# Kernel optimization log

Measured on AMD Instinct MI355X. Metric: run time of the kernel, lower is better.

Reference implementation:

```python
import jax, jax.numpy as jnp
import numpy as np

C = 64      # in_channels
D = 64      # hidden_dim (= per-head out dim since concat=False)
H = 4       # heads
N1 = 20000
N2 = 20000
E = 320000
NEG_SLOPE = 0.2


def setup_inputs() -> dict:
    key = jax.random.key(0)
    ks = jax.random.split(key, 32)
    inp = {}
    inp['x1'] = jax.random.normal(ks[0], (N1, C), dtype=jnp.float32)
    inp['x2'] = jax.random.normal(ks[1], (N2, C), dtype=jnp.float32)
    inp['edge_index1'] = jax.random.randint(ks[2], (2, E), 0, N1, dtype=jnp.int64)
    inp['edge_index2'] = jax.random.randint(ks[3], (2, E), 0, N2, dtype=jnp.int64)
    i = 4
    for tag in ['0', '1', '2', 'f']:
        inp['W' + tag] = jax.random.normal(ks[i], (H * D, C), dtype=jnp.float32) / np.sqrt(C); i += 1
        inp['as' + tag] = jax.random.normal(ks[i], (H, D), dtype=jnp.float32) * 0.1; i += 1
        inp['ad' + tag] = jax.random.normal(ks[i], (H, D), dtype=jnp.float32) * 0.1; i += 1
        inp['b' + tag] = jax.random.normal(ks[i], (C,), dtype=jnp.float32) * 0.02; i += 1
    inp['Wr'] = jax.random.normal(ks[i], (C, C), dtype=jnp.float32) / np.sqrt(C); i += 1
    inp['br'] = jax.random.normal(ks[i], (C,), dtype=jnp.float32) * 0.02
    return inp


def _build_edges(edge_index1, edge_index2, n1, n2):
    """Eval-mode combined edge list: e1 | e2+n1 | e1+n1, coalesced (dedup),
    then self-loops replaced with the full set (PyG GATConv behavior).
    Host-side numpy since edge dedup is data-dependent."""
    e1 = np.asarray(edge_index1)
    e2 = np.asarray(edge_index2) + n1
    e1o = e1 + n1  # edge_manipulator eval path: offset then mask (always valid here)
    valid = (e1o[0] < n1 + n2) & (e1o[1] < n1 + n2)
    e1o = e1o[:, valid]
    comb = np.concatenate([e1, e2, e1o], axis=1)
    comb = np.unique(comb, axis=1)  # coalesce: sort + dedup
    n = n1 + n2
    comb = comb[:, comb[0] != comb[1]]  # remove self loops
    loops = np.arange(n, dtype=comb.dtype)
    src = np.concatenate([comb[0], loops])
    dst = np.concatenate([comb[1], loops])
    return jnp.asarray(src), jnp.asarray(dst)


def gat(h_in, src, dst, n, W, a_s, a_d, b):
    # PyG GATConv, concat=False: mean over heads, bias of size out_channels.
    h = (h_in @ W.T).reshape(n, H, -1)                    # [N,H,D]
    asrc = jnp.einsum('nhd,hd->nh', h, a_s)               # [N,H]
    adst = jnp.einsum('nhd,hd->nh', h, a_d)
    e = jax.nn.leaky_relu(asrc[src] + adst[dst], NEG_SLOPE)  # [E,H]
    m = jax.ops.segment_max(e, dst, num_segments=n)
    ex = jnp.exp(e - m[dst])
    s = jax.ops.segment_sum(ex, dst, num_segments=n)
    alpha = ex / (s[dst] + 1e-16)                         # segment softmax over in-edges
    out = jax.ops.segment_sum(alpha[:, :, None] * h[src], dst, num_segments=n)  # [N,H,D]
    return out.mean(axis=1) + b


def reference(x1, x2, edge_index1, edge_index2,
              W0, as0, ad0, b0, W1, as1, ad1, b1, W2, as2, ad2, b2,
              Wf, asf, adf, bf, Wr, br):
    n1, n2 = x1.shape[0], x2.shape[0]
    n = n1 + n2
    src, dst = _build_edges(edge_index1, edge_index2, n1, n2)

    residual = x2 @ Wr.T + br
    h = jnp.concatenate([x1, x2], axis=0)
    # stacked layers (run under no_grad in torch; same forward math, eval dropout = identity)
    for (W, a_s, a_d, b) in [(W0, as0, ad0, b0), (W1, as1, ad1, b1), (W2, as2, ad2, b2)]:
        h = jax.nn.relu(gat(h, src, dst, n, W, a_s, a_d, b))
    h = gat(h, src, dst, n, Wf, asf, adf, bf)

    h2 = h[n1:n1 + n2]
    norm = jnp.linalg.norm(h2, axis=1, keepdims=True)
    h2n = h2 / jnp.maximum(norm, 1e-12)  # F.normalize(p=2, dim=1)
    return h2n + residual
```

## Files before the change

kernel.cpp:

```cpp
#include <hip/hip_runtime.h>

#define N1V 20000
#define N2V 20000
#define NU  20000
#define NUP 20032
#define EV  320000
#define CAP 128
#define SCB ((NU + 255) / 256)
#define BMW 640

typedef _Float16 f16x8 __attribute__((ext_vector_type(8)));
typedef float    f32x4 __attribute__((ext_vector_type(4)));
typedef float    f32x2 __attribute__((ext_vector_type(2)));

__device__ __forceinline__ unsigned short f2h_bits(float f){
  return __builtin_bit_cast(unsigned short, (_Float16)f);
}

__device__ __forceinline__ unsigned char f2fp8(float f){
#if __has_builtin(__builtin_amdgcn_cvt_pk_fp8_f32)
  int pk = __builtin_amdgcn_cvt_pk_fp8_f32(f, 0.f, 0, false);
  return (unsigned char)(pk & 0xff);
#else
  float a = fabsf(f);
  unsigned sgn = (f < 0.f) ? 0x80u : 0u;
  if (!(a == a)) return (unsigned char)(sgn | 0x7f);
  if (a < 7.8125e-3f) return (unsigned char)sgn;
  if (a > 448.f) a = 448.f;
  unsigned u = __float_as_uint(a);
  int e = (int)((u >> 23) & 0xff) - 127;
  unsigned m = (u >> 20) & 7u;
  unsigned rest = u & 0xfffffu;
  if (rest > 0x80000u || (rest == 0x80000u && (m & 1u))){ m++; if (m == 8u){ m = 0u; e++; } }
  if (e < -6) return (unsigned char)sgn;
  if (e > 8){ e = 8; m = 7u; }
  return (unsigned char)(sgn | ((unsigned)(e + 7) << 3) | m);
#endif
}

template<bool HI>
__device__ __forceinline__ f32x2 fp8pair(unsigned v){
#if __has_builtin(__builtin_amdgcn_cvt_pk_f32_fp8)
  auto t = __builtin_amdgcn_cvt_pk_f32_fp8((int)v, HI);
  return __builtin_bit_cast(f32x2, t);
#else
  unsigned b0 = (v >> (HI ? 16 : 0)) & 0xffu, b1 = (v >> (HI ? 24 : 8)) & 0xffu;
  auto one = [](unsigned b)->float{
    unsigned s = b & 0x80u, ef = (b >> 3) & 15u, m = b & 7u;
    float mag = ef ? __uint_as_float(((ef + 120u) << 23) | (m << 20))
                   : (float)m * 0.001953125f;
    return s ? -mag : mag;
  };
  f32x2 r = {one(b0), one(b1)};
  return r;
#endif
}

__global__ __launch_bounds__(256) void zero_init(unsigned* __restrict__ c1,
                                                 unsigned* __restrict__ c2,
                                                 unsigned* __restrict__ flag){
  int i = blockIdx.x*256 + threadIdx.x;
  if (i < NU){ c1[i] = 0u; c2[i] = 0u; }
  if (i == 0) *flag = 0u;
}

__global__ void detect_dtype(const unsigned* __restrict__ e, unsigned* __restrict__ flag){
  unsigned v = e[2*threadIdx.x + 1];
  if (v) atomicOr(flag, 1u);
}

__device__ __forceinline__ int rd_idx(const void* p, long long i, bool is64){
  return is64 ? (int)((const long long*)p)[i] : ((const int*)p)[i];
}

__global__ void scatter_buckets(const void* e1, const void* e2, const unsigned* __restrict__ flag,
                                unsigned* __restrict__ c1, unsigned* __restrict__ c2,
                                unsigned short* __restrict__ bA, unsigned short* __restrict__ bB){
  int i = blockIdx.x*blockDim.x + threadIdx.x;
  if (i >= 2*EV) return;
  bool is64 = (*flag == 0u);
  if (i < EV){
    int s = rd_idx(e1, i, is64), d = rd_idx(e1, (long long)EV+i, is64);
    if (s != d){
      unsigned p1 = atomicAdd(&c1[d], 1u);
      if (p1 < CAP) bA[(size_t)d*CAP + p1] = (unsigned short)s;
    }
  } else {
    int j = i - EV;
    int s = rd_idx(e2, j, is64), d = rd_idx(e2, (long long)EV+j, is64);
    if (s != d){
      unsigned p2 = atomicAdd(&c2[d], 1u);
      if (p2 < CAP) bB[(size_t)d*CAP + p2] = (unsigned short)s;
    }
  }
}

__device__ __forceinline__ unsigned row_raw(const unsigned* c1, const unsigned* c2, int i){
  unsigned a = c1[i]; if (a > CAP) a = CAP;
  unsigned b = c2[i]; if (b > CAP) b = CAP;
  return a + b + 1u;
}

__global__ __launch_bounds__(256) void scan_part(const unsigned* __restrict__ c1,
                                                 const unsigned* __restrict__ c2,
                                                 unsigned* __restrict__ bsum){
  int i = blockIdx.x*256 + threadIdx.x;
  unsigned v = (i < NU) ? row_raw(c1, c2, i) : 0u;
  #pragma unroll
  for (int off=32; off; off>>=1) v += __shfl_xor((int)v, off);
  __shared__ unsigned ws4[4];
  if ((threadIdx.x & 63) == 0) ws4[threadIdx.x >> 6] = v;
  __syncthreads();
  if (threadIdx.x == 0) bsum[blockIdx.x] = ws4[0]+ws4[1]+ws4[2]+ws4[3];
}

__global__ __launch_bounds__(256) void scan_final(const unsigned* __restrict__ c1,
                                                  const unsigned* __restrict__ c2,
                                                  const unsigned* __restrict__ bsum,
                                                  unsigned* __restrict__ rowoff){
  __shared__ unsigned lds[256];
  __shared__ unsigned ws4[4];
  int b = blockIdx.x, t = threadIdx.x;
  unsigned bv = (t < b) ? bsum[t] : 0u;
  #pragma unroll
  for (int off=32; off; off>>=1) bv += __shfl_xor((int)bv, off);
  if ((t & 63) == 0) ws4[t >> 6] = bv;
  __syncthreads();
  unsigned base = ws4[0]+ws4[1]+ws4[2]+ws4[3];
  int i = b*256 + t;
  unsigned v = (i < NU) ? row_raw(c1, c2, i) : 0u;
  lds[t] = v; __syncthreads();
  #pragma unroll
  for (int off=1; off<256; off<<=1){
    unsigned x = (t >= off) ? lds[t-off] : 0u;
    __syncthreads();
    lds[t] += x;
    __syncthreads();
  }
  unsigned excl = lds[t] - v + base;
  if (i < NU) rowoff[i] = excl;
  if (i == NU-1) rowoff[NU] = excl + v;
}

__global__ __launch_bounds__(256) void dedup_rows(
    const unsigned short* __restrict__ bA, const unsigned short* __restrict__ bB,
    const unsigned* __restrict__ c1, const unsigned* __restrict__ c2,
    const unsigned* __restrict__ rowoff, unsigned* __restrict__ csr,
    unsigned* __restrict__ rowcnt)
{
  __shared__ unsigned bm[4][BMW];
  int w = threadIdx.x >> 6, lane = threadIdx.x & 63;
  int t = blockIdx.x*4 + w;
  unsigned* bmw = bm[w];
  #pragma unroll
  for (int i = lane; i < BMW; i += 64) bmw[i] = 0u;
  __syncthreads();

  unsigned b = rowoff[t];
  unsigned a = c1[t]; if (a > CAP) a = CAP;
  unsigned bb = c2[t]; if (bb > CAP) bb = CAP;
  int nA = (int)a, nB = (int)bb;
  const unsigned short* rA = &bA[(size_t)t*CAP];
  const unsigned short* rB = &bB[(size_t)t*CAP];
  int cnt = nA + nB;
  int wc = 0;
  for (int i0 = 0; i0 < cnt; i0 += 64){
    int i = i0 + lane;
    bool act = (i < cnt);
    unsigned v = 0u;
    if (act) v = (i < nA) ? (unsigned)rA[i] : (unsigned)rB[i - nA];
    bool keep = false;
    if (act){
      unsigned bit = 1u << (v & 31u);
      unsigned old = atomicOr(&bmw[v >> 5], bit);
      keep = (old & bit) == 0u;
    }
    unsigned long long mask = __ballot(keep);
    int pos = wc + (int)__popcll(mask & ((1ull << lane) - 1ull));
    if (keep) csr[b + (unsigned)pos] = v;
    wc += (int)__popcll(mask);
  }
  if (lane == 0){
    csr[b + (unsigned)wc] = (unsigned)t;
    rowcnt[t] = (unsigned)(wc + 1);
  }
}

__global__ __launch_bounds__(256) void gemm_hp(
    const float* __restrict__ hin, const float* __restrict__ x2,
    const float* __restrict__ W,
    const float* __restrict__ a_s, const float* __restrict__ a_d,
    unsigned char* __restrict__ hp8, float* __restrict__ asv, float* __restrict__ adv)
{
  __shared__ __align__(16) unsigned short As[64][72];
  __shared__ __align__(16) unsigned short Bs[256][72];
  int tid = threadIdx.x;
  int nb  = blockIdx.x * 64;
  for (int i = tid; i < 256*64; i += 256)
    Bs[i>>6][i&63] = f2h_bits(W[i]);
  const float* src = hin ? hin : x2;
  for (int i = tid; i < 64*64; i += 256){
    int r = i>>6, c = i&63;
    int gn = nb + r; if (gn >= NU) gn = NU-1;
    As[r][c] = f2h_bits(src[(size_t)gn*64 + c]);
  }
  __syncthreads();

  int w = tid >> 6, lane = tid & 63;
  int fr = lane & 15, fq = lane >> 4;
  int wc = w * 64;
  const f32x4 zero = {0.f, 0.f, 0.f, 0.f};
  f32x4 acc[4][4];
  #pragma unroll
  for (int a=0; a<4; ++a)
    #pragma unroll
    for (int b=0; b<4; ++b) acc[a][b] = zero;

  #pragma unroll
  for (int ks=0; ks<2; ++ks){
    int k0 = ks*32 + fq*8;
    f16x8 af[4], bfv[4];
    #pragma unroll
    for (int rt=0; rt<4; ++rt) af[rt]  = *(const f16x8*)&As[rt*16 + fr][k0];
    #pragma unroll
    for (int ct=0; ct<4; ++ct) bfv[ct] = *(const f16x8*)&Bs[wc + ct*16 + fr][k0];
    #pragma unroll
    for (int rt=0; rt<4; ++rt)
      #pragma unroll
      for (int ct=0; ct<4; ++ct)
        acc[rt][ct] = __builtin_amdgcn_mfma_f32_16x16x32_f16(af[rt], bfv[ct], acc[rt][ct], 0, 0, 0);
  }

  #pragma unroll
  for (int rt=0; rt<4; ++rt)
    #pragma unroll
    for (int ct=0; ct<4; ++ct)
      #pragma unroll
      for (int j=0; j<4; ++j){
        int gn = nb + rt*16 + fq*4 + j;
        int o  = wc + ct*16 + fr;
        hp8[(size_t)gn*256 + ((o & 63) << 2) + (o >> 6)] = f2fp8(acc[rt][ct][j]);
      }

  float asr[4], adr[4];
  #pragma unroll
  for (int ct=0; ct<4; ++ct){
    asr[ct] = a_s[wc + ct*16 + fr];
    adr[ct] = a_d[wc + ct*16 + fr];
  }
  #pragma unroll
  for (int rt=0; rt<4; ++rt)
    #pragma unroll
    for (int j=0; j<4; ++j){
      float ps = acc[rt][0][j]*asr[0] + acc[rt][1][j]*asr[1]
               + acc[rt][2][j]*asr[2] + acc[rt][3][j]*asr[3];
      float pd = acc[rt][0][j]*adr[0] + acc[rt][1][j]*adr[1]
               + acc[rt][2][j]*adr[2] + acc[rt][3][j]*adr[3];
      #pragma unroll
      for (int off=1; off<16; off<<=1){
        ps += __shfl_xor(ps, off);
        pd += __shfl_xor(pd, off);
      }
      if (fr == 0){
        int gn = nb + rt*16 + fq*4 + j;
        asv[(size_t)gn*4 + w] = ps;
        adv[(size_t)gn*4 + w] = pd;
      }
    }
}

template<int MODE>
__global__ __launch_bounds__(256) void gat_aggr8(
    const unsigned* __restrict__ csr, const unsigned* __restrict__ rowoff,
    const unsigned* __restrict__ rowcnt, const unsigned char* __restrict__ hp8,
    const float* __restrict__ asv, const float* __restrict__ adv,
    const float* __restrict__ bias, float* __restrict__ hout,
    const float* __restrict__ resid, float* __restrict__ outp)
{
  __shared__ __align__(16) float4 wbuf[4][64];
  int w    = threadIdx.x >> 6;
  int lane = threadIdx.x & 63;
  int dst  = blockIdx.x*4 + w;
  unsigned base = rowoff[dst];
  int cnt = (int)rowcnt[dst];
  float4 adn = *(const float4*)&adv[(size_t)dst*4];
  float4* wrow = wbuf[w];

  f32x2 accA = {0.f, 0.f}, accB = {0.f, 0.f};
  float ss0=0.f, ss1=0.f, ss2=0.f, ss3=0.f;

#define GATHER1(J) { \
    int su = __builtin_amdgcn_readlane(sv, (J)); \
    float4 wv = wrow[(J)]; \
    unsigned hv = *(const unsigned*)(hp8 + (((size_t)(unsigned)su) << 8) + (lane << 2)); \
    f32x2 h01 = fp8pair<false>(hv); \
    f32x2 h23 = fp8pair<true>(hv); \
    f32x2 w01 = {wv.x, wv.y}, w23 = {wv.z, wv.w}; \
    accA += h01 * w01; \
    accB += h23 * w23; }

  for (int i0=0; i0<cnt; i0+=64){
    int i = i0 + lane;
    int sv = 0; float x0=0.f, x1=0.f, x2v=0.f, x3=0.f;
    if (i < cnt){
      sv = (int)csr[base + i];
      float4 a = *(const float4*)&asv[(size_t)sv*4];
      float e0 = a.x + adn.x; e0 = e0 > 0.f ? e0 : 0.2f*e0; x0  = __expf(e0 - 4.f);
      float e1 = a.y + adn.y; e1 = e1 > 0.f ? e1 : 0.2f*e1; x1  = __expf(e1 - 4.f);
      float e2 = a.z + adn.z; e2 = e2 > 0.f ? e2 : 0.2f*e2; x2v = __expf(e2 - 4.f);
      float e3 = a.w + adn.w; e3 = e3 > 0.f ? e3 : 0.2f*e3; x3  = __expf(e3 - 4.f);
      ss0 += x0; ss1 += x1; ss2 += x2v; ss3 += x3;
    }
    float4 wpk = {x0, x1, x2v, x3};
    wrow[lane] = wpk;
    __builtin_amdgcn_wave_barrier();
    int lim = cnt - i0; if (lim > 64) lim = 64;
    int lim8 = (lim + 7) & ~7;
    for (int j = 0; j < lim8; j += 8){
      GATHER1(j)
      GATHER1(j+1)
      GATHER1(j+2)
      GATHER1(j+3)
      GATHER1(j+4)
      GATHER1(j+5)
      GATHER1(j+6)
      GATHER1(j+7)
    }
    __builtin_amdgcn_wave_barrier();
  }
#undef GATHER1

  #pragma unroll
  for (int off=32; off; off>>=1){
    ss0 += __shfl_xor(ss0, off); ss1 += __shfl_xor(ss1, off);
    ss2 += __shfl_xor(ss2, off); ss3 += __shfl_xor(ss3, off);
  }
  float r = 0.25f*( accA.x/(ss0 + 1e-16f) + accA.y/(ss1 + 1e-16f)
                  + accB.x/(ss2 + 1e-16f) + accB.y/(ss3 + 1e-16f) ) + bias[lane];
  if (MODE == 0){
    r = fmaxf(r, 0.f);
    hout[(size_t)dst*64 + lane] = r;
  } else {
    float ssq = r*r;
    #pragma unroll
    for (int off=32; off; off>>=1) ssq += __shfl_xor(ssq, off);
    float sc = 1.f / fmaxf(sqrtf(ssq), 1e-12f);
    size_t o = (size_t)dst*64 + lane;
    outp[o] = r*sc + resid[o];
  }
}

__global__ __launch_bounds__(256) void resid_gemm(const float* __restrict__ x2,
    const float* __restrict__ Wr, const float* __restrict__ br, float* __restrict__ resid){
  __shared__ float WT[64][65];
  int tid = threadIdx.x;
  for (int i = tid; i < 64*64; i += 256) WT[i & 63][i >> 6] = Wr[i];
  __syncthreads();
  int row = blockIdx.x*4 + (tid >> 6);
  int c   = tid & 63;
  const float* xr = &x2[(size_t)row*64];
  float acc = br[c];
  #pragma unroll 8
  for (int k=0; k<64; ++k) acc = fmaf(xr[k], WT[k][c], acc);
  resid[(size_t)row*64 + c] = acc;
}

extern "C" void kernel_launch(void* const* d_in, const int* in_sizes, int n_in,
                              void* d_out, int out_size, void* d_ws, size_t ws_size,
                              hipStream_t stream)
{
  (void)in_sizes; (void)n_in; (void)out_size; (void)ws_size;
  const float* x2  = (const float*)d_in[1];
  const void*  ei1 = d_in[2];
  const void*  ei2 = d_in[3];
  const float* Wm[4] = {(const float*)d_in[4],  (const float*)d_in[8],
                        (const float*)d_in[12], (const float*)d_in[16]};
  const float* Asv[4] = {(const float*)d_in[5],  (const float*)d_in[9],
                         (const float*)d_in[13], (const float*)d_in[17]};
  const float* Adv[4] = {(const float*)d_in[6],  (const float*)d_in[10],
                         (const float*)d_in[14], (const float*)d_in[18]};
  const float* Bv[4]  = {(const float*)d_in[7],  (const float*)d_in[11],
                         (const float*)d_in[15], (const float*)d_in[19]};
  const float* Wr = (const float*)d_in[20];
  const float* br = (const float*)d_in[21];
  float* out = (float*)d_out;

  char* p = (char*)d_ws;
  auto alloc = [&](size_t b){ void* r = (void*)p; p += (b + 1023) & ~(size_t)1023; return r; };
  unsigned* c1      = (unsigned*)alloc((size_t)NU*4);
  unsigned* c2      = (unsigned*)alloc((size_t)NU*4);
  unsigned* rowoff  = (unsigned*)alloc((size_t)(NU+1)*4);
  unsigned* rowcnt  = (unsigned*)alloc((size_t)NU*4);
  unsigned* bsum    = (unsigned*)alloc((size_t)SCB*4);
  unsigned* csr     = (unsigned*)alloc((size_t)(2*EV + NU)*4);
  unsigned short* bA = (unsigned short*)alloc((size_t)NU*CAP*2);
  unsigned short* bB = (unsigned short*)alloc((size_t)NU*CAP*2);
  unsigned char* hp8 = (unsigned char*)alloc((size_t)NUP*256);
  float* asv   = (float*)alloc((size_t)NUP*4*4);
  float* adv   = (float*)alloc((size_t)NUP*4*4);
  float* bufA  = (float*)alloc((size_t)NUP*64*4);
  float* bufB  = (float*)alloc((size_t)NUP*64*4);
  float* resid = (float*)alloc((size_t)N2V*64*4);
  unsigned* flag = (unsigned*)alloc(4);

  zero_init<<<SCB, 256, 0, stream>>>(c1, c2, flag);
  detect_dtype<<<1, 256, 0, stream>>>((const unsigned*)ei1, flag);
  scatter_buckets<<<(2*EV + 255)/256, 256, 0, stream>>>(ei1, ei2, flag, c1, c2, bA, bB);
  scan_part<<<SCB, 256, 0, stream>>>(c1, c2, bsum);
  scan_final<<<SCB, 256, 0, stream>>>(c1, c2, bsum, rowoff);
  dedup_rows<<<NU/4, 256, 0, stream>>>(bA, bB, c1, c2, rowoff, csr, rowcnt);
  resid_gemm<<<N2V/4, 256, 0, stream>>>(x2, Wr, br, resid);

  const float* hin = nullptr;
  float* houts[3] = {bufA, bufB, bufA};
  for (int l = 0; l < 3; ++l){
    gemm_hp<<<NUP/64, 256, 0, stream>>>(hin, x2, Wm[l], Asv[l], Adv[l], hp8, asv, adv);
    gat_aggr8<0><<<NU/4, 256, 0, stream>>>(csr, rowoff, rowcnt, hp8, asv, adv, Bv[l],
                                           houts[l], nullptr, nullptr);
    hin = houts[l];
  }
  gemm_hp<<<NUP/64, 256, 0, stream>>>(hin, x2, Wm[3], Asv[3], Adv[3], hp8, asv, adv);
  gat_aggr8<2><<<NU/4, 256, 0, stream>>>(csr, rowoff, rowcnt, hp8, asv, adv, Bv[3],
                                         nullptr, resid, out);
}
```

Measured before the change: 240.7 us.

## Replace CSR build with in-place deduped fixed-stride uint16 buckets

Drops the two prefix-scan kernels and the separate 32-bit CSR array. Each destination row now lives in a fixed-stride 16-bit bucket (272 slots) that is deduplicated in place, and the aggregation kernels read neighbor indices straight from it. The per-row counters are spaced 16 words apart to cut atomic contention on shared cache lines. This saves two kernel launches and halves the bytes per index read in the four aggregation passes. In exchange it uses a larger, padded bucket footprint, and a larger counter array must be zeroed.

Result: faster. 229.0 us (-4.9%).

```diff
diff --git a/kernel.cpp b/kernel.cpp
--- a/kernel.cpp
+++ b/kernel.cpp
@@ -6,7 +6,8 @@
 #define NUP 20032
 #define EV  320000
 #define CAP 128
-#define SCB ((NU + 255) / 256)
+#define CSTR 16
+#define BSTR 272
 #define BMW 640
 
 typedef _Float16 f16x8 __attribute__((ext_vector_type(8)));
@@ -60,7 +61,7 @@
                                                  unsigned* __restrict__ c2,
                                                  unsigned* __restrict__ flag){
   int i = blockIdx.x*256 + threadIdx.x;
-  if (i < NU){ c1[i] = 0u; c2[i] = 0u; }
+  if (i < NU*CSTR){ c1[i] = 0u; c2[i] = 0u; }
   if (i == 0) *flag = 0u;
 }
 
@@ -75,77 +76,29 @@
 
 __global__ void scatter_buckets(const void* e1, const void* e2, const unsigned* __restrict__ flag,
                                 unsigned* __restrict__ c1, unsigned* __restrict__ c2,
-                                unsigned short* __restrict__ bA, unsigned short* __restrict__ bB){
+                                unsigned short* __restrict__ bucket){
   int i = blockIdx.x*blockDim.x + threadIdx.x;
   if (i >= 2*EV) return;
   bool is64 = (*flag == 0u);
   if (i < EV){
     int s = rd_idx(e1, i, is64), d = rd_idx(e1, (long long)EV+i, is64);
     if (s != d){
-      unsigned p1 = atomicAdd(&c1[d], 1u);
-      if (p1 < CAP) bA[(size_t)d*CAP + p1] = (unsigned short)s;
+      unsigned p = atomicAdd(&c1[(size_t)d*CSTR], 1u);
+      if (p < CAP) bucket[(size_t)d*BSTR + p] = (unsigned short)s;
     }
   } else {
     int j = i - EV;
     int s = rd_idx(e2, j, is64), d = rd_idx(e2, (long long)EV+j, is64);
     if (s != d){
-      unsigned p2 = atomicAdd(&c2[d], 1u);
-      if (p2 < CAP) bB[(size_t)d*CAP + p2] = (unsigned short)s;
-    }
-  }
-}
-
-__device__ __forceinline__ unsigned row_raw(const unsigned* c1, const unsigned* c2, int i){
-  unsigned a = c1[i]; if (a > CAP) a = CAP;
-  unsigned b = c2[i]; if (b > CAP) b = CAP;
-  return a + b + 1u;
-}
-
-__global__ __launch_bounds__(256) void scan_part(const unsigned* __restrict__ c1,
-                                                 const unsigned* __restrict__ c2,
-                                                 unsigned* __restrict__ bsum){
-  int i = blockIdx.x*256 + threadIdx.x;
-  unsigned v = (i < NU) ? row_raw(c1, c2, i) : 0u;
-  #pragma unroll
-  for (int off=32; off; off>>=1) v += __shfl_xor((int)v, off);
-  __shared__ unsigned ws4[4];
-  if ((threadIdx.x & 63) == 0) ws4[threadIdx.x >> 6] = v;
-  __syncthreads();
-  if (threadIdx.x == 0) bsum[blockIdx.x] = ws4[0]+ws4[1]+ws4[2]+ws4[3];
-}
-
-__global__ __launch_bounds__(256) void scan_final(const unsigned* __restrict__ c1,
-                                                  const unsigned* __restrict__ c2,
-                                                  const unsigned* __restrict__ bsum,
-                                                  unsigned* __restrict__ rowoff){
-  __shared__ unsigned lds[256];
-  __shared__ unsigned ws4[4];
-  int b = blockIdx.x, t = threadIdx.x;
-  unsigned bv = (t < b) ? bsum[t] : 0u;
-  #pragma unroll
-  for (int off=32; off; off>>=1) bv += __shfl_xor((int)bv, off);
-  if ((t & 63) == 0) ws4[t >> 6] = bv;
-  __syncthreads();
-  unsigned base = ws4[0]+ws4[1]+ws4[2]+ws4[3];
-  int i = b*256 + t;
-  unsigned v = (i < NU) ? row_raw(c1, c2, i) : 0u;
-  lds[t] = v; __syncthreads();
-  #pragma unroll
-  for (int off=1; off<256; off<<=1){
-    unsigned x = (t >= off) ? lds[t-off] : 0u;
-    __syncthreads();
-    lds[t] += x;
-    __syncthreads();
-  }
-  unsigned excl = lds[t] - v + base;
-  if (i < NU) rowoff[i] = excl;
-  if (i == NU-1) rowoff[NU] = excl + v;
+      unsigned p = atomicAdd(&c2[(size_t)d*CSTR], 1u);
+      if (p < CAP) bucket[(size_t)d*BSTR + CAP + p] = (unsigned short)s;
+    }
+  }
 }
 
 __global__ __launch_bounds__(256) void dedup_rows(
-    const unsigned short* __restrict__ bA, const unsigned short* __restrict__ bB,
+    unsigned short* __restrict__ bucket,
     const unsigned* __restrict__ c1, const unsigned* __restrict__ c2,
-    const unsigned* __restrict__ rowoff, unsigned* __restrict__ csr,
     unsigned* __restrict__ rowcnt)
 {
   __shared__ unsigned bm[4][BMW];
@@ -156,19 +109,17 @@
   for (int i = lane; i < BMW; i += 64) bmw[i] = 0u;
   __syncthreads();
 
-  unsigned b = rowoff[t];
-  unsigned a = c1[t]; if (a > CAP) a = CAP;
-  unsigned bb = c2[t]; if (bb > CAP) bb = CAP;
+  unsigned a = c1[(size_t)t*CSTR]; if (a > CAP) a = CAP;
+  unsigned bb = c2[(size_t)t*CSTR]; if (bb > CAP) bb = CAP;
   int nA = (int)a, nB = (int)bb;
-  const unsigned short* rA = &bA[(size_t)t*CAP];
-  const unsigned short* rB = &bB[(size_t)t*CAP];
+  unsigned short* row = &bucket[(size_t)t*BSTR];
   int cnt = nA + nB;
   int wc = 0;
   for (int i0 = 0; i0 < cnt; i0 += 64){
     int i = i0 + lane;
     bool act = (i < cnt);
     unsigned v = 0u;
-    if (act) v = (i < nA) ? (unsigned)rA[i] : (unsigned)rB[i - nA];
+    if (act) v = (i < nA) ? (unsigned)row[i] : (unsigned)row[CAP + (i - nA)];
     bool keep = false;
     if (act){
       unsigned bit = 1u << (v & 31u);
@@ -177,11 +128,11 @@
     }
     unsigned long long mask = __ballot(keep);
     int pos = wc + (int)__popcll(mask & ((1ull << lane) - 1ull));
-    if (keep) csr[b + (unsigned)pos] = v;
+    if (keep) row[pos] = (unsigned short)v;
     wc += (int)__popcll(mask);
   }
   if (lane == 0){
-    csr[b + (unsigned)wc] = (unsigned)t;
+    row[wc] = (unsigned short)t;
     rowcnt[t] = (unsigned)(wc + 1);
   }
 }
@@ -271,8 +222,8 @@
 
 template<int MODE>
 __global__ __launch_bounds__(256) void gat_aggr8(
-    const unsigned* __restrict__ csr, const unsigned* __restrict__ rowoff,
-    const unsigned* __restrict__ rowcnt, const unsigned char* __restrict__ hp8,
+    const unsigned short* __restrict__ bucket, const unsigned* __restrict__ rowcnt,
+    const unsigned char* __restrict__ hp8,
     const float* __restrict__ asv, const float* __restrict__ adv,
     const float* __restrict__ bias, float* __restrict__ hout,
     const float* __restrict__ resid, float* __restrict__ outp)
@@ -281,7 +232,7 @@
   int w    = threadIdx.x >> 6;
   int lane = threadIdx.x & 63;
   int dst  = blockIdx.x*4 + w;
-  unsigned base = rowoff[dst];
+  const unsigned short* row = &bucket[(size_t)dst*BSTR];
   int cnt = (int)rowcnt[dst];
   float4 adn = *(const float4*)&adv[(size_t)dst*4];
   float4* wrow = wbuf[w];
@@ -303,7 +254,7 @@
     int i = i0 + lane;
     int sv = 0; float x0=0.f, x1=0.f, x2v=0.f, x3=0.f;
     if (i < cnt){
-      sv = (int)csr[base + i];
+      sv = (int)row[i];
       float4 a = *(const float4*)&asv[(size_t)sv*4];
       float e0 = a.x + adn.x; e0 = e0 > 0.f ? e0 : 0.2f*e0; x0  = __expf(e0 - 4.f);
       float e1 = a.y + adn.y; e1 = e1 > 0.f ? e1 : 0.2f*e1; x1  = __expf(e1 - 4.f);
@@ -387,14 +338,10 @@
 
   char* p = (char*)d_ws;
   auto alloc = [&](size_t b){ void* r = (void*)p; p += (b + 1023) & ~(size_t)1023; return r; };
-  unsigned* c1      = (unsigned*)alloc((size_t)NU*4);
-  unsigned* c2      = (unsigned*)alloc((size_t)NU*4);
-  unsigned* rowoff  = (unsigned*)alloc((size_t)(NU+1)*4);
+  unsigned* c1      = (unsigned*)alloc((size_t)NU*CSTR*4);
+  unsigned* c2      = (unsigned*)alloc((size_t)NU*CSTR*4);
   unsigned* rowcnt  = (unsigned*)alloc((size_t)NU*4);
-  unsigned* bsum    = (unsigned*)alloc((size_t)SCB*4);
-  unsigned* csr     = (unsigned*)alloc((size_t)(2*EV + NU)*4);
-  unsigned short* bA = (unsigned short*)alloc((size_t)NU*CAP*2);
-  unsigned short* bB = (unsigned short*)alloc((size_t)NU*CAP*2);
+  unsigned short* bucket = (unsigned short*)alloc((size_t)NU*BSTR*2);
   unsigned char* hp8 = (unsigned char*)alloc((size_t)NUP*256);
   float* asv   = (float*)alloc((size_t)NUP*4*4);
   float* adv   = (float*)alloc((size_t)NUP*4*4);
@@ -403,23 +350,21 @@
   float* resid = (float*)alloc((size_t)N2V*64*4);
   unsigned* flag = (unsigned*)alloc(4);
 
-  zero_init<<<SCB, 256, 0, stream>>>(c1, c2, flag);
+  zero_init<<<(NU*CSTR + 255)/256, 256, 0, stream>>>(c1, c2, flag);
   detect_dtype<<<1, 256, 0, stream>>>((const unsigned*)ei1, flag);
-  scatter_buckets<<<(2*EV + 255)/256, 256, 0, stream>>>(ei1, ei2, flag, c1, c2, bA, bB);
-  scan_part<<<SCB, 256, 0, stream>>>(c1, c2, bsum);
-  scan_final<<<SCB, 256, 0, stream>>>(c1, c2, bsum, rowoff);
-  dedup_rows<<<NU/4, 256, 0, stream>>>(bA, bB, c1, c2, rowoff, csr, rowcnt);
+  scatter_buckets<<<(2*EV + 255)/256, 256, 0, stream>>>(ei1, ei2, flag, c1, c2, bucket);
+  dedup_rows<<<NU/4, 256, 0, stream>>>(bucket, c1, c2, rowcnt);
   resid_gemm<<<N2V/4, 256, 0, stream>>>(x2, Wr, br, resid);
 
   const float* hin = nullptr;
   float* houts[3] = {bufA, bufB, bufA};
   for (int l = 0; l < 3; ++l){
     gemm_hp<<<NUP/64, 256, 0, stream>>>(hin, x2, Wm[l], Asv[l], Adv[l], hp8, asv, adv);
-    gat_aggr8<0><<<NU/4, 256, 0, stream>>>(csr, rowoff, rowcnt, hp8, asv, adv, Bv[l],
+    gat_aggr8<0><<<NU/4, 256, 0, stream>>>(bucket, rowcnt, hp8, asv, adv, Bv[l],
                                            houts[l], nullptr, nullptr);
     hin = houts[l];
   }
   gemm_hp<<<NUP/64, 256, 0, stream>>>(hin, x2, Wm[3], Asv[3], Adv[3], hp8, asv, adv);
-  gat_aggr8<2><<<NU/4, 256, 0, stream>>>(csr, rowoff, rowcnt, hp8, asv, adv, Bv[3],
+  gat_aggr8<2><<<NU/4, 256, 0, stream>>>(bucket, rowcnt, hp8, asv, adv, Bv[3],
                                          nullptr, resid, out);
 }
```
